# Optimization experiments

Hardware: AMD Instinct MI355X
Metric: run time of the kernel (lower is better)

The kernel has to match this reference:

```python
import jax, jax.numpy as jnp
import numpy as np

B, M, N = 512, 196, 77
FEAT, NUM_CLASSES = 512, 632
TEXT_DIM, LOCAL_DIM = 768, 576
EPS_OT, MAX_ITER, THRESH = 0.1, 100, 0.01
MARGIN, LS_EPS, TEMP, BN_EPS = 0.3, 0.1, 2.0, 1e-5
W_TEACHER = W_STUDENT = W_GLOBAL = W_LOCAL = 1.0


def setup_inputs() -> dict:
    key = jax.random.key(0)
    ks = jax.random.split(key, 16)
    nrm = lambda k, s, sc=0.02: (jax.random.normal(k, s, jnp.float32) * sc)
    return {
        "text_feat": jax.random.normal(ks[0], (B, N, TEXT_DIM), jnp.float32),
        "teacher_image_raw": jax.random.normal(ks[1], (B, TEXT_DIM), jnp.float32),
        "student_global_raw": jax.random.normal(ks[2], (B, LOCAL_DIM), jnp.float32),
        "student_local_feat": jax.random.normal(ks[3], (B, M, LOCAL_DIM), jnp.float32),
        "label": jax.random.randint(ks[4], (B,), 0, NUM_CLASSES),
        "W_tv": nrm(ks[5], (FEAT, TEXT_DIM)), "b_tv": jnp.zeros((FEAT,), jnp.float32),
        "W_tt": nrm(ks[6], (LOCAL_DIM, TEXT_DIM)), "b_tt": jnp.zeros((LOCAL_DIM,), jnp.float32),
        "W_sv": nrm(ks[7], (FEAT, LOCAL_DIM)), "b_sv": jnp.zeros((FEAT,), jnp.float32),
        "tv_bn_g": jnp.ones((FEAT,), jnp.float32), "tv_bn_b": jnp.zeros((FEAT,), jnp.float32),
        "W_cls_t": nrm(ks[8], (NUM_CLASSES, FEAT)), "b_cls_t": jnp.zeros((NUM_CLASSES,), jnp.float32),
        "W_cls_s": nrm(ks[9], (NUM_CLASSES, FEAT)), "b_cls_s": jnp.zeros((NUM_CLASSES,), jnp.float32),
    }


def batchnorm_train(x, g, b):
    mu = jnp.mean(x, axis=0)
    var = jnp.var(x, axis=0)
    return (x - mu) * jax.lax.rsqrt(var + BN_EPS) * g + b


def ce_label_smooth(logits, label):
    logp = jax.nn.log_softmax(logits, axis=-1)
    onehot = jax.nn.one_hot(label, NUM_CLASSES, dtype=logits.dtype)
    q = (1.0 - LS_EPS) * onehot + LS_EPS / NUM_CLASSES
    return -jnp.mean(jnp.sum(q * logp, axis=-1))


def triplet_hard(feat, label):
    sq = jnp.sum(feat * feat, axis=1)
    d2 = sq[:, None] + sq[None, :] - 2.0 * (feat @ feat.T)
    dist = jnp.sqrt(jnp.clip(d2, 1e-12, None))
    pos = label[:, None] == label[None, :]
    dist_ap = jnp.max(jnp.where(pos, dist, -jnp.inf), axis=1)   # hardest positive
    dist_an = jnp.min(jnp.where(pos, jnp.inf, dist), axis=1)    # hardest negative
    return jnp.mean(jax.nn.relu(dist_ap - dist_an + MARGIN))    # margin ranking, y=1


def distill_kl(teacher_logits, student_logits):
    t_logp = jax.nn.log_softmax(teacher_logits / TEMP, axis=1)
    s_logp = jax.nn.log_softmax(student_logits / TEMP, axis=1)
    t = jnp.exp(t_logp)
    return jnp.sum(t * (t_logp - s_logp)) / teacher_logits.shape[0]  # batchmean


def sinkhorn(K, u, v):
    # device-side convergence check replaces torch's .item() host sync
    def cond(st):
        i, r, c, err = st
        return jnp.logical_and(i < MAX_ITER, err >= THRESH)

    def body(st):
        i, r, c, _ = st
        r0 = r
        r = u / jnp.einsum('bmn,bn->bm', K, c)
        c = v / jnp.einsum('bmn,bm->bn', K, r)
        return (i + 1, r, c, jnp.mean(jnp.abs(r - r0)))

    r = jnp.ones_like(u)
    c = jnp.ones_like(v)
    init = (jnp.int32(0), r, c, jnp.array(jnp.inf, K.dtype))
    _, r, c, _ = jax.lax.while_loop(cond, body, init)
    return r[:, :, None] * c[:, None, :] * K


def ot_loss(student_local, teacher_text):
    s = student_local / jnp.clip(jnp.linalg.norm(student_local, axis=-1, keepdims=True), 1e-12)
    t = teacher_text / jnp.clip(jnp.linalg.norm(teacher_text, axis=-1, keepdims=True), 1e-12)
    sim = jnp.einsum('bmd,bnd->bmn', s, t)
    wdist = 1.0 - sim
    xx = jnp.full((sim.shape[0], sim.shape[1]), 1.0 / sim.shape[1], sim.dtype)
    yy = jnp.full((sim.shape[0], sim.shape[2]), 1.0 / sim.shape[2], sim.dtype)
    KK = jnp.exp(-wdist / EPS_OT)
    T = jax.lax.stop_gradient(sinkhorn(KK, xx, yy))  # torch.no_grad block
    sim_op = jnp.sum(T * sim, axis=(1, 2))
    return 1.0 - jnp.mean(sim_op)


def reference(text_feat, teacher_image_raw, student_global_raw, student_local_feat,
              label, W_tv, b_tv, W_tt, b_tt, W_sv, b_sv, tv_bn_g, tv_bn_b,
              W_cls_t, b_cls_t, W_cls_s, b_cls_s):
    teacher_image_feat = batchnorm_train(teacher_image_raw @ W_tv.T + b_tv, tv_bn_g, tv_bn_b)
    teacher_text_feat = text_feat @ W_tt.T + b_tt            # (B, N, 576)
    student_global_feat = student_global_raw @ W_sv.T + b_sv  # (B, FEAT)

    teacher_logits = teacher_image_feat @ W_cls_t.T + b_cls_t
    loss_teacher = ce_label_smooth(teacher_logits, label) + triplet_hard(teacher_image_feat, label)

    student_logits = student_global_feat @ W_cls_s.T + b_cls_s
    loss_student = ce_label_smooth(student_logits, label) + triplet_hard(student_global_feat, label)

    preds = jnp.argmax(student_logits, axis=1)
    loss_global = distill_kl(teacher_logits, student_logits)
    loss_local = ot_loss(student_local_feat, teacher_text_feat)

    loss = (W_LOCAL * loss_local + W_GLOBAL * loss_global
            + W_TEACHER * loss_teacher + W_STUDENT * loss_student)
    return loss, preds
```

## Files before the change

kernel.cpp:

```cpp
#include <hip/hip_runtime.h>
#include <math.h>

#define B_     512
#define M_     196
#define N_     77
#define FEAT_  512
#define NCLS_  632
#define TDIM_  768
#define LDIM_  576
#define LS_EPS_ 0.1f
#define MARGIN_ 0.3f
#define BN_EPS_ 1e-5f
#define SINK_ITERS 12

typedef float fx4 __attribute__((ext_vector_type(4)));
typedef float fx8 __attribute__((ext_vector_type(8)));
typedef short sx8 __attribute__((ext_vector_type(8)));
typedef __bf16 bfx8 __attribute__((ext_vector_type(8)));

__device__ inline ushort f2bf(float f) {
  union { float f; uint u; } v; v.f = f;
  uint u = v.u;
  return (ushort)((u + 0x7FFFu + ((u >> 16) & 1u)) >> 16);
}
__device__ inline float bf2f(ushort b) {
  union { uint u; float f; } v; v.u = ((uint)b) << 16;
  return v.f;
}
__device__ inline sx8 cvt8(fx8 f) {
  bfx8 h = __builtin_convertvector(f, bfx8);
  return __builtin_bit_cast(sx8, h);
}
__device__ inline fx8 b2f8(sx8 s) {
  bfx8 h = __builtin_bit_cast(bfx8, s);
  return __builtin_convertvector(h, fx8);
}
__device__ inline fx4 mfma16(sx8 a, sx8 b, fx4 c) {
  return __builtin_amdgcn_mfma_f32_16x16x32_bf16(
      __builtin_bit_cast(bfx8, a), __builtin_bit_cast(bfx8, b), c, 0, 0, 0);
}
__device__ inline void gload_lds16(const void* g, void* l) {
  auto gp = (const __attribute__((address_space(1))) uint*)(uintptr_t)g;
  auto lp = (__attribute__((address_space(3))) uint*)(uintptr_t)l;
  __builtin_amdgcn_global_load_lds(gp, lp, 16, 0, 0);
}


__device__ inline void small_mfma_body(char* smem, int bx, int by,
                                       const float* __restrict__ A,
                                       const float* __restrict__ Wm,
                                       const float* __restrict__ bias,
                                       float* __restrict__ C, int N, int K) {
  ushort* ldsA = (ushort*)smem;
  ushort* ldsW = (ushort*)(smem + 4096);
  const int tid = threadIdx.x;
  const int lane = tid & 63;
  const int wv = tid >> 6;
  const int wr = wv >> 1, wc = wv & 1;
  const int row0 = by * 64;
  const int col0 = bx * 64;
  const int mt = tid >> 6;
  const int l16 = lane & 15;
  const int k8 = lane >> 4;

  const float* pA = A + (size_t)(row0 + mt * 16 + l16) * K + k8 * 8;
  int wcl = col0 + mt * 16 + l16;
  if (wcl >= N) wcl = N - 1;
  const float* pW = Wm + (size_t)wcl * K + k8 * 8;

  fx4 acc[2][2];
  const fx4 zz = {0.f, 0.f, 0.f, 0.f};
  acc[0][0] = zz; acc[0][1] = zz; acc[1][0] = zz; acc[1][1] = zz;

  sx8 ua = cvt8(*(const fx8*)pA);
  sx8 uw = cvt8(*(const fx8*)pW);
  const int NT = K >> 5;
  for (int kt = 0; kt < NT; ++kt) {
    if (kt) __syncthreads();
    *(sx8*)&ldsA[tid * 8] = ua;
    *(sx8*)&ldsW[tid * 8] = uw;
    __syncthreads();
    if (kt + 1 < NT) {
      ua = cvt8(*(const fx8*)(pA + (kt + 1) * 32));
      uw = cvt8(*(const fx8*)(pW + (kt + 1) * 32));
    }
    sx8 af[2], bf[2];
#pragma unroll
    for (int mi = 0; mi < 2; ++mi) af[mi] = *(sx8*)&ldsA[((wr * 2 + mi) * 64 + lane) * 8];
#pragma unroll
    for (int ni = 0; ni < 2; ++ni) bf[ni] = *(sx8*)&ldsW[((wc * 2 + ni) * 64 + lane) * 8];
#pragma unroll
    for (int mi = 0; mi < 2; ++mi)
#pragma unroll
      for (int ni = 0; ni < 2; ++ni) acc[mi][ni] = mfma16(af[mi], bf[ni], acc[mi][ni]);
  }
#pragma unroll
  for (int mi = 0; mi < 2; ++mi) {
    int rbase = row0 + (wr * 2 + mi) * 16 + ((lane >> 4) << 2);
#pragma unroll
    for (int ni = 0; ni < 2; ++ni) {
      int col = col0 + (wc * 2 + ni) * 16 + l16;
      if (col < N) {
        float bv = bias ? bias[col] : 0.f;
#pragma unroll
        for (int r = 0; r < 4; ++r)
          C[(size_t)(rbase + r) * N + col] = acc[mi][ni][r] + bv;
      }
    }
  }
}

__device__ inline void gemm_nt32_body(char* smem, int bx, int by,
                                      const float* __restrict__ A,
                                      const float* __restrict__ W,
                                      const float* __restrict__ bias,
                                      float* __restrict__ C, int Mr, int N, int K) {
  float (*As)[33] = (float (*)[33])smem;
  float (*Ws)[33] = (float (*)[33])(smem + 4224);
  const int tid = threadIdx.x;
  const int tx = tid & 15, ty = tid >> 4;
  const int row0 = by * 32;
  const int col0 = bx * 32;
  float acc[2][2] = {{0.f, 0.f}, {0.f, 0.f}};

  for (int k0 = 0; k0 < K; k0 += 32) {
#pragma unroll
    for (int e = tid; e < 32 * 32; e += 256) {
      int r = e / 32, c = e % 32;
      int gr = row0 + r, gc = k0 + c;
      As[r][c] = (gr < Mr && gc < K) ? A[(size_t)gr * K + gc] : 0.f;
    }
#pragma unroll
    for (int e = tid; e < 32 * 32; e += 256) {
      int r = e / 32, c = e % 32;
      int gr = col0 + r, gc = k0 + c;
      Ws[r][c] = (gr < N && gc < K) ? W[(size_t)gr * K + gc] : 0.f;
    }
    __syncthreads();
#pragma unroll
    for (int kk = 0; kk < 32; ++kk) {
      float a[2], wv[2];
#pragma unroll
      for (int i = 0; i < 2; ++i) a[i] = As[ty * 2 + i][kk];
#pragma unroll
      for (int j = 0; j < 2; ++j) wv[j] = Ws[tx * 2 + j][kk];
#pragma unroll
      for (int i = 0; i < 2; ++i)
#pragma unroll
        for (int j = 0; j < 2; ++j) acc[i][j] += a[i] * wv[j];
    }
    __syncthreads();
  }
#pragma unroll
  for (int i = 0; i < 2; ++i) {
    int gr = row0 + ty * 2 + i;
    if (gr >= Mr) continue;
#pragma unroll
    for (int j = 0; j < 2; ++j) {
      int gc = col0 + tx * 2 + j;
      if (gc >= N) continue;
      float v = acc[i][j];
      if (bias) v += bias[gc];
      C[(size_t)gr * N + gc] = v;
    }
  }
}

__device__ inline void bn_body(char* pool, int j,
                               const float* __restrict__ X, float* __restrict__ Y,
                               const float* __restrict__ g, const float* __restrict__ b) {
  const int tid = threadIdx.x;
  float* sf = (float*)pool;
  float vals[2];
  float s = 0.f, s2 = 0.f;
  int idx = 0;
  for (int i = tid; i < B_; i += 256, ++idx) {
    float v = X[(size_t)i * FEAT_ + j];
    vals[idx] = v;
    s += v; s2 += v * v;
  }
  sf[tid] = s; __syncthreads();
  for (int k = 128; k > 0; k >>= 1) { if (tid < k) sf[tid] += sf[tid + k]; __syncthreads(); }
  float mu = sf[0] * (1.f / B_); __syncthreads();
  sf[tid] = s2; __syncthreads();
  for (int k = 128; k > 0; k >>= 1) { if (tid < k) sf[tid] += sf[tid + k]; __syncthreads(); }
  float var = sf[0] * (1.f / B_) - mu * mu;
  float scale = rsqrtf(var + BN_EPS_) * g[j];
  float shift = b[j];
  idx = 0;
  for (int i = tid; i < B_; i += 256, ++idx)
    Y[(size_t)i * FEAT_ + j] = (vals[idx] - mu) * scale + shift;
}

__device__ inline void ce_kl_body(char* pool, int row,
                                  const float* __restrict__ TL,
                                  const float* __restrict__ SL,
                                  const int* __restrict__ label,
                                  float* __restrict__ acc,
                                  float* __restrict__ preds) {
  const int tid = threadIdx.x;
  const float* tp = TL + (size_t)row * NCLS_;
  const float* sp = SL + (size_t)row * NCLS_;
  float (*red)[256] = (float (*)[256])pool;
  int* ridx = (int*)(pool + 4096);
  float* sxl = (float*)(pool + 5120);

  float tv[3], sv[3];
#pragma unroll
  for (int k = 0; k < 3; ++k) {
    int j = tid + k * 256;
    tv[k] = (j < NCLS_) ? tp[j] : -INFINITY;
    sv[k] = (j < NCLS_) ? sp[j] : -INFINITY;
  }
  float mT = -INFINITY, mS = -INFINITY, sT = 0.f, sS = 0.f;
  int ai = NCLS_;
#pragma unroll
  for (int k = 0; k < 3; ++k) {
    int j = tid + k * 256;
    if (j < NCLS_) {
      mT = fmaxf(mT, tv[k]);
      sT += tv[k]; sS += sv[k];
      if (sv[k] > mS) { mS = sv[k]; ai = j; }
    }
  }
  red[0][tid] = mT; red[1][tid] = mS; red[2][tid] = sT; red[3][tid] = sS; ridx[tid] = ai;
  __syncthreads();
  for (int k = 128; k > 0; k >>= 1) {
    if (tid < k) {
      red[0][tid] = fmaxf(red[0][tid], red[0][tid + k]);
      float om = red[1][tid + k]; int oi = ridx[tid + k];
      if (om > red[1][tid] || (om == red[1][tid] && oi < ridx[tid])) { red[1][tid] = om; ridx[tid] = oi; }
      red[2][tid] += red[2][tid + k];
      red[3][tid] += red[3][tid + k];
    }
    __syncthreads();
  }
  const float MT = red[0][0], MS = red[1][0], sumT = red[2][0], sumS = red[3][0];
  const int amax = ridx[0];
  __syncthreads();
  float etr = 0.f, esr = 0.f, eth = 0.f, esh = 0.f;
#pragma unroll
  for (int k = 0; k < 3; ++k) {
    int j = tid + k * 256;
    if (j < NCLS_) {
      etr += expf(tv[k] - MT);
      esr += expf(sv[k] - MS);
      eth += expf(0.5f * (tv[k] - MT));
      esh += expf(0.5f * (sv[k] - MS));
    }
  }
  red[0][tid] = etr; red[1][tid] = esr; red[2][tid] = eth; red[3][tid] = esh;
  __syncthreads();
  for (int k = 128; k > 0; k >>= 1) {
    if (tid < k) {
      red[0][tid] += red[0][tid + k];
      red[1][tid] += red[1][tid + k];
      red[2][tid] += red[2][tid + k];
      red[3][tid] += red[3][tid + k];
    }
    __syncthreads();
  }
  const float lseT = MT + logf(red[0][0]);
  const float lseS = MS + logf(red[1][0]);
  const float ltH = 0.5f * MT + logf(red[2][0]);
  const float lsH = 0.5f * MS + logf(red[3][0]);
  __syncthreads();
  const int lab = label[row];
  float klp = 0.f;
#pragma unroll
  for (int k = 0; k < 3; ++k) {
    int j = tid + k * 256;
    if (j < NCLS_) {
      float tlp = 0.5f * tv[k] - ltH;
      float slp = 0.5f * sv[k] - lsH;
      klp += expf(tlp) * (tlp - slp);
      if (j == lab) { sxl[0] = tv[k]; sxl[1] = sv[k]; }
    }
  }
  red[0][tid] = klp;
  __syncthreads();
  for (int k = 128; k > 0; k >>= 1) {
    if (tid < k) red[0][tid] += red[0][tid + k];
    __syncthreads();
  }
  if (tid == 0) {
    float ce_t = -((1.f - LS_EPS_) * (sxl[0] - lseT) + (LS_EPS_ / NCLS_) * (sumT - NCLS_ * lseT));
    float ce_s = -((1.f - LS_EPS_) * (sxl[1] - lseS) + (LS_EPS_ / NCLS_) * (sumS - NCLS_ * lseS));
    atomicAdd(acc + 0, ce_t * (1.f / B_));
    atomicAdd(acc + 2, ce_s * (1.f / B_));
    atomicAdd(acc + 4, red[0][0] * (1.f / B_));
    preds[row] = (float)amax;
  }
}

__device__ inline void triplet_body(char* pool, int which, int i,
                                    const float* __restrict__ Gt,
                                    const float* __restrict__ Gs,
                                    const int* __restrict__ label,
                                    float* __restrict__ acc) {
  const float* G = which ? Gs : Gt;
  float* a = acc + (which ? 3 : 1);
  const int tid = threadIdx.x;
  const int li = label[i];
  float* sap = (float*)pool;
  float* san = (float*)(pool + 1024);
  const float sqi = G[(size_t)i * B_ + i];
  float ap = -INFINITY, an = INFINITY;
  for (int j = tid; j < B_; j += 256) {
    float sqj = G[(size_t)j * B_ + j];
    float d2 = sqi + sqj - 2.f * G[(size_t)i * B_ + j];
    float d = sqrtf(fmaxf(d2, 1e-12f));
    if (label[j] == li) ap = fmaxf(ap, d); else an = fminf(an, d);
  }
  sap[tid] = ap; san[tid] = an; __syncthreads();
  for (int k = 128; k > 0; k >>= 1) {
    if (tid < k) {
      sap[tid] = fmaxf(sap[tid], sap[tid + k]);
      san[tid] = fminf(san[tid], san[tid + k]);
    }
    __syncthreads();
  }
  if (tid == 0) atomicAdd(a, fmaxf(sap[0] - san[0] + MARGIN_, 0.f) * (1.f / B_));
}

#define SKLD 88
#define SKTLD 200
__device__ inline void sinkhorn_body(char* pool, int b,
                                     const ushort* __restrict__ sim,
                                     float* __restrict__ acc) {
  const int tid = threadIdx.x;
  ushort* Kb  = (ushort*)pool;
  ushort* KbT = (ushort*)(pool + 34496);
  float* r    = (float*)(pool + 65296);
  float* c    = (float*)(pool + 66080);
  float* sf   = (float*)(pool + 66432);
  float* cs1  = (float*)(pool + 67456);
  const ushort* simb = sim + (size_t)b * (M_ * N_);
  for (int e = tid; e < 196 * SKLD; e += 256) {
    int m = e / SKLD, n = e - m * SKLD;
    if (n < 77) {
      float sv = bf2f(simb[m * 77 + n]);
      ushort h = f2bf(__expf((sv - 1.f) * 10.f));
      Kb[e] = h;
      KbT[n * SKTLD + m] = h;
    } else Kb[e] = 0;
  }
  if (tid < SKLD) c[tid] = (tid < 77) ? 1.f : 0.f;
  __syncthreads();
  const float uu = 1.f / 196.f, vv = 1.f / 77.f;
  for (int it = 0; it < SINK_ITERS; ++it) {
    if (tid < 196) {
      const ushort* Km = &Kb[tid * SKLD];
      float s = 0.f;
#pragma unroll
      for (int j = 0; j < 11; ++j) {
        fx8 kf = b2f8(*(const sx8*)&Km[j * 8]);
#pragma unroll
        for (int q = 0; q < 8; ++q) s += kf[q] * c[j * 8 + q];
      }
      r[tid] = uu / s;
    }
    __syncthreads();
    if (tid < 154) {
      const int half = (tid >= 77) ? 1 : 0;
      const int n = tid - 77 * half;
      const ushort* Kn = &KbT[n * SKTLD + 96 * half];
      const int m0 = 96 * half;
      float s = 0.f;
#pragma unroll
      for (int j = 0; j < 12; ++j) {
        fx8 kf = b2f8(*(const sx8*)&Kn[j * 8]);
#pragma unroll
        for (int q = 0; q < 8; ++q) s += kf[q] * r[m0 + j * 8 + q];
      }
      if (half) {
        s += bf2f(Kn[96]) * r[192] + bf2f(Kn[97]) * r[193]
           + bf2f(Kn[98]) * r[194] + bf2f(Kn[99]) * r[195];
        cs1[n] = s;
      } else sf[n] = s;
    }
    __syncthreads();
    if (tid < 77) c[tid] = vv / (sf[tid] + cs1[tid]);
    __syncthreads();
  }
  float part = 0.f;
  for (int e = tid; e < M_ * N_; e += 256) {
    int m = e / 77, n = e - m * 77;
    part += r[m] * c[n] * bf2f(Kb[m * SKLD + n]) * bf2f(simb[e]);
  }
  sf[tid] = part; __syncthreads();
  for (int k = 128; k > 0; k >>= 1) { if (tid < k) sf[tid] += sf[tid + k]; __syncthreads(); }
  if (tid == 0) atomicAdd(acc + 5, sf[0] * (1.f / B_));
}

template<int H>
__device__ void sim_body(int b, const float* __restrict__ S, const ushort* __restrict__ T,
                         ushort* __restrict__ sim, ushort* lds, float* sinv_s, float* tinv_s) {
  constexpr int NTILE = (H == 2) ? 5 : 4;
  constexpr int NS = NTILE * 64;
  constexpr int NC = NS + 320;
  constexpr int M0 = H * 64;
  const int tid = threadIdx.x;
  const int lane = tid & 63;
  const int w = tid >> 6;

  bool val[3], isS[3];
  const float* pS[3];
  const ushort* pT[3];
  int rowi[3], cidx[3];
  bool k0lane[3];
#pragma unroll
  for (int j = 0; j < 3; ++j) {
    int c = tid + j * 256;
    cidx[j] = c;
    val[j] = (c < NC);
    isS[j] = (c < NS);
    k0lane[j] = (((c >> 4) & 3) == 0);
    if (c < NS) {
      int tile = c >> 6;
      int r = M0 + tile * 16 + (c & 15);
      int rr = r < 196 ? r : 195;
      int ks = ((c >> 4) & 3) * 8;
      pS[j] = S + ((size_t)b * M_ + rr) * LDIM_ + ks;
      rowi[j] = rr - M0;
      pT[j] = T;
    } else {
      int cc = c - NS;
      int tile = cc >> 6;
      int r = tile * 16 + (cc & 15);
      int rr = r < 77 ? r : 76;
      int ks = ((cc >> 4) & 3) * 8;
      pT[j] = T + ((size_t)b * N_ + rr) * LDIM_ + ks;
      pS[j] = S;
      rowi[j] = rr;
    }
  }

  fx8 fS[3]; sx8 tS[3];
#pragma unroll
  for (int j = 0; j < 3; ++j) {
    if (!val[j]) continue;
    if (isS[j]) fS[j] = *(const fx8*)pS[j];
    else tS[j] = *(const sx8*)pT[j];
  }

  float ss[3] = {0.f, 0.f, 0.f};
  fx4 acc[2][5];
  const fx4 zz = {0.f, 0.f, 0.f, 0.f};
#pragma unroll
  for (int i = 0; i < 2; ++i)
#pragma unroll
    for (int j = 0; j < 5; ++j) acc[i][j] = zz;

  for (int kt = 0; kt < 18; ++kt) {
    if (kt) __syncthreads();
#pragma unroll
    for (int j = 0; j < 3; ++j) {
      if (!val[j]) continue;
      if (isS[j]) {
        *(sx8*)&lds[cidx[j] * 8] = cvt8(fS[j]);
#pragma unroll
        for (int q = 0; q < 8; ++q) ss[j] += fS[j][q] * fS[j][q];
      } else {
        *(sx8*)&lds[cidx[j] * 8] = tS[j];
        fx8 tf = b2f8(tS[j]);
#pragma unroll
        for (int q = 0; q < 8; ++q) ss[j] += tf[q] * tf[q];
      }
    }
    __syncthreads();
    if (kt < 17) {
      const int ko = (kt + 1) * 32;
#pragma unroll
      for (int j = 0; j < 3; ++j) {
        if (!val[j]) continue;
        if (isS[j]) fS[j] = *(const fx8*)(pS[j] + ko);
        else tS[j] = *(const sx8*)(pT[j] + ko);
      }
    }
    sx8 bfr[5];
#pragma unroll
    for (int ni = 0; ni < 5; ++ni) bfr[ni] = *(sx8*)&lds[(NS + ni * 64 + lane) * 8];
#pragma unroll
    for (int mi = 0; mi < 2; ++mi) {
      int lt = w + mi * 4;
      if (lt < NTILE) {
        sx8 af = *(sx8*)&lds[(lt * 64 + lane) * 8];
#pragma unroll
        for (int ni = 0; ni < 5; ++ni) acc[mi][ni] = mfma16(af, bfr[ni], acc[mi][ni]);
      }
    }
  }

#pragma unroll
  for (int j = 0; j < 3; ++j) {
    if (!val[j]) continue;
    float s = ss[j];
    s += __shfl_xor(s, 16);
    s += __shfl_xor(s, 32);
    if (k0lane[j]) {
      float inv = 1.f / fmaxf(sqrtf(s), 1e-12f);
      if (isS[j]) sinv_s[rowi[j]] = inv;
      else        tinv_s[rowi[j]] = inv;
    }
  }
  __syncthreads();

#pragma unroll
  for (int mi = 0; mi < 2; ++mi) {
    int lt = w + mi * 4;
    if (lt >= NTILE) continue;
    int lrbase = lt * 16 + ((lane >> 4) << 2);
#pragma unroll
    for (int ni = 0; ni < 5; ++ni) {
      int col = ni * 16 + (lane & 15);
      if (col < 77) {
        float tv = tinv_s[col];
#pragma unroll
        for (int r = 0; r < 4; ++r) {
          int lrow = lrbase + r;
          int row = M0 + lrow;
          if (row < 196)
            sim[((size_t)b * M_ + row) * N_ + col] = f2bf(acc[mi][ni][r] * sinv_s[lrow] * tv);
        }
      }
    }
  }
}

__device__ inline void gemm128_body(char* pool, int bx, int by,
                                    const ushort* __restrict__ A,
                                    const ushort* __restrict__ Bm,
                                    const float* __restrict__ bias,
                                    ushort* __restrict__ C) {
  ushort* ldsA = (ushort*)pool;
  ushort* ldsB = (ushort*)(pool + 8192);
  const int tid = threadIdx.x;
  const int lane = tid & 63;
  const int w = tid >> 6;
  const int wr = w >> 1, wc = w & 1;
  const int row0 = by * 128;
  const int col0 = bx * 128;
  const int l16 = lane & 15, k8 = (lane >> 4) * 8;

  const ushort* gA0 = A + (size_t)(row0 + (2 * w) * 16 + l16) * TDIM_ + k8;
  const ushort* gA1 = A + (size_t)(row0 + (2 * w + 1) * 16 + l16) * TDIM_ + k8;
  const ushort* gB0 = Bm + (size_t)(col0 + (2 * w) * 16 + l16) * TDIM_ + k8;
  const ushort* gB1 = Bm + (size_t)(col0 + (2 * w + 1) * 16 + l16) * TDIM_ + k8;
  ushort* lA0 = &ldsA[(2 * w) * 512];
  ushort* lA1 = &ldsA[(2 * w + 1) * 512];
  ushort* lB0 = &ldsB[(2 * w) * 512];
  ushort* lB1 = &ldsB[(2 * w + 1) * 512];

  fx4 acc[4][4];
  const fx4 zz = {0.f, 0.f, 0.f, 0.f};
#pragma unroll
  for (int i = 0; i < 4; ++i)
#pragma unroll
    for (int j = 0; j < 4; ++j) acc[i][j] = zz;

  for (int kt = 0; kt < 24; ++kt) {
    if (kt) __syncthreads();
    const int ko = kt * 32;
    gload_lds16(gA0 + ko, lA0);
    gload_lds16(gA1 + ko, lA1);
    gload_lds16(gB0 + ko, lB0);
    gload_lds16(gB1 + ko, lB1);
    asm volatile("s_waitcnt vmcnt(0)" ::: "memory");
    __syncthreads();
    sx8 af[4], bf[4];
#pragma unroll
    for (int mi = 0; mi < 4; ++mi) af[mi] = *(sx8*)&ldsA[((wr * 4 + mi) * 64 + lane) * 8];
#pragma unroll
    for (int ni = 0; ni < 4; ++ni) bf[ni] = *(sx8*)&ldsB[((wc * 4 + ni) * 64 + lane) * 8];
#pragma unroll
    for (int mi = 0; mi < 4; ++mi)
#pragma unroll
      for (int ni = 0; ni < 4; ++ni) acc[mi][ni] = mfma16(af[mi], bf[ni], acc[mi][ni]);
  }

#pragma unroll
  for (int mi = 0; mi < 4; ++mi) {
    int rbase = row0 + wr * 64 + mi * 16 + ((lane >> 4) << 2);
#pragma unroll
    for (int ni = 0; ni < 4; ++ni) {
      int col = col0 + wc * 64 + ni * 16 + l16;
      if (col < 576) {
        float bv = bias[col];
#pragma unroll
        for (int r = 0; r < 4; ++r)
          C[(size_t)(rbase + r) * 576 + col] = f2bf(acc[mi][ni][r] + bv);
      }
    }
  }
}


__global__ __launch_bounds__(256) void kernel_A(const float* __restrict__ t_img_raw,
                                                const float* __restrict__ W_tv,
                                                const float* __restrict__ b_tv,
                                                float* __restrict__ tlin,
                                                const float* __restrict__ s_glob_raw,
                                                const float* __restrict__ W_sv,
                                                const float* __restrict__ b_sv,
                                                float* __restrict__ sglob,
                                                const float* __restrict__ W_tt,
                                                ushort* __restrict__ Wbuf,
                                                float* __restrict__ acc,
                                                const float* __restrict__ text_feat,
                                                ushort* __restrict__ Abuf) {
  __shared__ __align__(16) char pool[8448];
  const int bid = blockIdx.x;
  const int tid = threadIdx.x;
  if (bid < 64) {
    small_mfma_body(pool, bid & 7, bid >> 3, t_img_raw, W_tv, b_tv, tlin, FEAT_, TDIM_);
  } else if (bid < 320) {
    int i = bid - 64;
    gemm_nt32_body(pool, i & 15, i >> 4, s_glob_raw, W_sv, b_sv, sglob, 512, FEAT_, LDIM_);
  } else if (bid < 561) {
    int pbid = bid - 320;
    if (pbid == 240) {
      if (tid < 8) acc[tid] = 0.f;
      return;
    }
    int i = pbid * 256 + tid;
    int row = i / 96;
    if (row < 576) {
      fx8 f = *(const fx8*)(W_tt + (size_t)i * 8);
      *(sx8*)(Wbuf + (size_t)i * 8) = cvt8(f);
    } else {
      sx8 z = {0, 0, 0, 0, 0, 0, 0, 0};
      *(sx8*)(Wbuf + (size_t)i * 8) = z;
    }
  } else {
    size_t i = (size_t)(bid - 561) * 256 + tid;
    fx8 f = *(const fx8*)(text_feat + i * 8);
    *(sx8*)(Abuf + i * 8) = cvt8(f);
  }
}

__global__ __launch_bounds__(256) void kernel_B(const ushort* __restrict__ Abuf,
                                                const ushort* __restrict__ Wbuf,
                                                const float* __restrict__ b_tt,
                                                ushort* __restrict__ ttext,
                                                const float* __restrict__ tlin,
                                                float* __restrict__ timg,
                                                const float* __restrict__ bn_g,
                                                const float* __restrict__ bn_b) {
  __shared__ __align__(16) char pool[16384];
  const int bid = blockIdx.x;
  if (bid < 1540) {
    const int xcd = bid & 7, wi = bid >> 3;
    const int swz = (xcd < 4 ? xcd * 193 : 772 + (xcd - 4) * 192) + wi;
    const int by = swz / 5, bx = swz - by * 5;
    gemm128_body(pool, bx, by, Abuf, Wbuf, b_tt, ttext);
  } else {
    bn_body(pool, bid - 1540, tlin, timg, bn_g, bn_b);
  }
}

__global__ __launch_bounds__(256) void kernel_C(const float* __restrict__ s_local,
                                                const ushort* __restrict__ ttext,
                                                ushort* __restrict__ sim,
                                                const float* __restrict__ timg,
                                                const float* __restrict__ W_ct,
                                                const float* __restrict__ b_ct,
                                                float* __restrict__ tlog,
                                                const float* __restrict__ sglob,
                                                const float* __restrict__ W_cs,
                                                const float* __restrict__ b_cs,
                                                float* __restrict__ slog,
                                                float* __restrict__ gram_t,
                                                float* __restrict__ gram_s) {
  __shared__ __align__(16) char pool[10880];
  const int bid = blockIdx.x;
  if (bid < 1536) {
    ushort* lds = (ushort*)pool;
    float* sinv_s = (float*)(pool + 10240);
    float* tinv_s = (float*)(pool + 10560);
    const int swz = (bid & 7) * 192 + (bid >> 3);
    const int b = swz / 3;
    const int q = swz - b * 3;
    if (q == 0)      sim_body<0>(b, s_local, ttext, sim, lds, sinv_s, tinv_s);
    else if (q == 1) sim_body<1>(b, s_local, ttext, sim, lds, sinv_s, tinv_s);
    else             sim_body<2>(b, s_local, ttext, sim, lds, sinv_s, tinv_s);
  } else {
    int i = bid - 1536;
    if (i < 80) {
      small_mfma_body(pool, i % 10, i / 10, timg, W_ct, b_ct, tlog, NCLS_, FEAT_);
    } else if (i < 400) {
      int j = i - 80;
      gemm_nt32_body(pool, j % 20, j / 20, sglob, W_cs, b_cs, slog, 512, NCLS_, FEAT_);
    } else if (i < 464) {
      int j = i - 400;
      small_mfma_body(pool, j & 7, j >> 3, timg, timg, nullptr, gram_t, 512, FEAT_);
    } else {
      int j = i - 464;
      small_mfma_body(pool, j & 7, j >> 3, sglob, sglob, nullptr, gram_s, 512, LDIM_);
    }
  }
}

__global__ __launch_bounds__(256) void kernel_D(const ushort* __restrict__ sim,
                                                const float* __restrict__ tlog,
                                                const float* __restrict__ slog,
                                                const float* __restrict__ gram_t,
                                                const float* __restrict__ gram_s,
                                                const int* __restrict__ label,
                                                float* __restrict__ acc,
                                                float* __restrict__ out) {
  __shared__ __align__(16) char pool[67840];
  const int bid = blockIdx.x;
  if (bid < 512) {
    sinkhorn_body(pool, bid, sim, acc);
  } else if (bid < 1024) {
    ce_kl_body(pool, bid - 512, tlog, slog, label, acc, out + 1);
  } else {
    int i = bid - 1024;
    triplet_body(pool, i >> 9, i & 511, gram_t, gram_s, label, acc);
  }
  if (threadIdx.x == 0) {
    __threadfence();
    uint prev = atomicAdd((uint*)(acc + 6), 1u);
    if (prev == 2047u) {
      float a0 = atomicAdd(acc + 0, 0.f);
      float a1 = atomicAdd(acc + 1, 0.f);
      float a2 = atomicAdd(acc + 2, 0.f);
      float a3 = atomicAdd(acc + 3, 0.f);
      float a4 = atomicAdd(acc + 4, 0.f);
      float a5 = atomicAdd(acc + 5, 0.f);
      out[0] = a0 + a1 + a2 + a3 + a4 + (1.f - a5);
    }
  }
}

extern "C" void kernel_launch(void* const* d_in, const int* in_sizes, int n_in,
                              void* d_out, int out_size, void* d_ws, size_t ws_size,
                              hipStream_t stream) {
  const float* text_feat  = (const float*)d_in[0];
  const float* t_img_raw  = (const float*)d_in[1];
  const float* s_glob_raw = (const float*)d_in[2];
  const float* s_local    = (const float*)d_in[3];
  const int*   label      = (const int*)d_in[4];
  const float* W_tv = (const float*)d_in[5];
  const float* b_tv = (const float*)d_in[6];
  const float* W_tt = (const float*)d_in[7];
  const float* b_tt = (const float*)d_in[8];
  const float* W_sv = (const float*)d_in[9];
  const float* b_sv = (const float*)d_in[10];
  const float* bn_g = (const float*)d_in[11];
  const float* bn_b = (const float*)d_in[12];
  const float* W_ct = (const float*)d_in[13];
  const float* b_ct = (const float*)d_in[14];
  const float* W_cs = (const float*)d_in[15];
  const float* b_cs = (const float*)d_in[16];
  float* out = (float*)d_out;
  float* ws = (float*)d_ws;

  float* tlin   = ws;
  float* timg   = tlin + 262144;
  float* sglob  = timg + 262144;
  float* tlog   = sglob + 262144;
  float* slog   = tlog + 323584;
  float* gram_t = slog + 323584;
  float* gram_s = gram_t + 262144;
  float* acc    = gram_s + 262144;
  ushort* Wbuf  = (ushort*)(acc + 8);
  ushort* ttext = Wbuf + 491520;
  ushort* Abuf  = ttext + 22708224;
  ushort* sim   = Abuf;

  dim3 blk(256);

  kernel_A<<<15345, blk, 0, stream>>>(t_img_raw, W_tv, b_tv, tlin,
                                      s_glob_raw, W_sv, b_sv, sglob,
                                      W_tt, Wbuf, acc, text_feat, Abuf);
  kernel_B<<<2052, blk, 0, stream>>>(Abuf, Wbuf, b_tt, ttext, tlin, timg, bn_g, bn_b);
  kernel_C<<<2064, blk, 0, stream>>>(s_local, ttext, sim,
                                     timg, W_ct, b_ct, tlog,
                                     sglob, W_cs, b_cs, slog, gram_t, gram_s);
  kernel_D<<<2048, blk, 0, stream>>>(sim, tlog, slog, gram_t, gram_s, label, acc, out);
}
```

Measured before the change: 408.2 us.

## Compute per-batch similarity in one block with text tile staged in LDS

The similarity GEMM used to be split over three blocks per batch item. It now runs in a single block per batch item. The text features are staged into LDS in two K-halves using direct global-to-LDS loads, and the student local features stream straight from global memory into registers for the MFMA. The text row norms are computed once per block. This cuts redundant text loads across blocks and the per-K-step LDS round trips and barriers. In exchange the grid has fewer blocks, LDS use grows to about 46KB, and the S loads are no longer prefetched, so occupancy and latency hiding may suffer.

```diff
diff --git a/kernel.cpp b/kernel.cpp
--- a/kernel.cpp
+++ b/kernel.cpp
@@ -393,135 +393,99 @@
   if (tid == 0) atomicAdd(acc + 5, sf[0] * (1.f / B_));
 }
 
-template<int H>
-__device__ void sim_body(int b, const float* __restrict__ S, const ushort* __restrict__ T,
-                         ushort* __restrict__ sim, ushort* lds, float* sinv_s, float* tinv_s) {
-  constexpr int NTILE = (H == 2) ? 5 : 4;
-  constexpr int NS = NTILE * 64;
-  constexpr int NC = NS + 320;
-  constexpr int M0 = H * 64;
+__device__ void sim_batch_body(int b, const float* __restrict__ S,
+                               const ushort* __restrict__ T,
+                               ushort* __restrict__ sim, char* pool) {
+  ushort* ldsT = (ushort*)pool;
+  float* tinv_s = (float*)(pool + 46080);
   const int tid = threadIdx.x;
   const int lane = tid & 63;
   const int w = tid >> 6;
-
-  bool val[3], isS[3];
-  const float* pS[3];
-  const ushort* pT[3];
-  int rowi[3], cidx[3];
-  bool k0lane[3];
-#pragma unroll
-  for (int j = 0; j < 3; ++j) {
-    int c = tid + j * 256;
-    cidx[j] = c;
-    val[j] = (c < NC);
-    isS[j] = (c < NS);
-    k0lane[j] = (((c >> 4) & 3) == 0);
-    if (c < NS) {
-      int tile = c >> 6;
-      int r = M0 + tile * 16 + (c & 15);
-      int rr = r < 196 ? r : 195;
-      int ks = ((c >> 4) & 3) * 8;
-      pS[j] = S + ((size_t)b * M_ + rr) * LDIM_ + ks;
-      rowi[j] = rr - M0;
-      pT[j] = T;
-    } else {
-      int cc = c - NS;
-      int tile = cc >> 6;
-      int r = tile * 16 + (cc & 15);
-      int rr = r < 77 ? r : 76;
-      int ks = ((cc >> 4) & 3) * 8;
-      pT[j] = T + ((size_t)b * N_ + rr) * LDIM_ + ks;
-      pS[j] = S;
-      rowi[j] = rr;
-    }
-  }
-
-  fx8 fS[3]; sx8 tS[3];
-#pragma unroll
-  for (int j = 0; j < 3; ++j) {
-    if (!val[j]) continue;
-    if (isS[j]) fS[j] = *(const fx8*)pS[j];
-    else tS[j] = *(const sx8*)pT[j];
-  }
-
-  float ss[3] = {0.f, 0.f, 0.f};
-  fx4 acc[2][5];
+  const int l16 = lane & 15;
+  const int khi = lane >> 4;
+  const float* Sb = S + (size_t)b * M_ * LDIM_;
+  const ushort* Tb = T + (size_t)b * N_ * LDIM_;
+
+  fx4 acc[4][5];
   const fx4 zz = {0.f, 0.f, 0.f, 0.f};
 #pragma unroll
-  for (int i = 0; i < 2; ++i)
-#pragma unroll
-    for (int j = 0; j < 5; ++j) acc[i][j] = zz;
-
-  for (int kt = 0; kt < 18; ++kt) {
-    if (kt) __syncthreads();
-#pragma unroll
-    for (int j = 0; j < 3; ++j) {
-      if (!val[j]) continue;
-      if (isS[j]) {
-        *(sx8*)&lds[cidx[j] * 8] = cvt8(fS[j]);
-#pragma unroll
-        for (int q = 0; q < 8; ++q) ss[j] += fS[j][q] * fS[j][q];
-      } else {
-        *(sx8*)&lds[cidx[j] * 8] = tS[j];
-        fx8 tf = b2f8(tS[j]);
-#pragma unroll
-        for (int q = 0; q < 8; ++q) ss[j] += tf[q] * tf[q];
+  for (int s = 0; s < 4; ++s)
+#pragma unroll
+    for (int ni = 0; ni < 5; ++ni) acc[s][ni] = zz;
+  float ss[4] = {0.f, 0.f, 0.f, 0.f};
+
+#pragma unroll
+  for (int p = 0; p < 2; ++p) {
+#pragma unroll
+    for (int j = 0; j < 12; ++j) {
+      int c = tid + j * 256;
+      if (c < 2880) {
+        int ktl = c / 320;
+        int rem = c - ktl * 320;
+        int nt = rem >> 6, cl = rem & 63;
+        int row = nt * 16 + (cl & 15);
+        if (row > 76) row = 76;
+        int k = (p * 9 + ktl) * 32 + ((cl >> 4) & 3) * 8;
+        gload_lds16(Tb + (size_t)row * LDIM_ + k, ldsT + (size_t)c * 8);
       }
     }
-    __syncthreads();
-    if (kt < 17) {
-      const int ko = (kt + 1) * 32;
-#pragma unroll
-      for (int j = 0; j < 3; ++j) {
-        if (!val[j]) continue;
-        if (isS[j]) fS[j] = *(const fx8*)(pS[j] + ko);
-        else tS[j] = *(const sx8*)(pT[j] + ko);
+    if (p == 0) {
+      for (int row = w; row < N_; row += 4) {
+        const ushort* x = Tb + (size_t)row * LDIM_;
+        float s = 0.f;
+#pragma unroll
+        for (int i = 0; i < 9; ++i) { float v = bf2f(x[lane + i * 64]); s += v * v; }
+#pragma unroll
+        for (int off = 32; off > 0; off >>= 1) s += __shfl_down(s, off);
+        if (lane == 0) tinv_s[row] = 1.f / fmaxf(sqrtf(s), 1e-12f);
       }
     }
-    sx8 bfr[5];
-#pragma unroll
-    for (int ni = 0; ni < 5; ++ni) bfr[ni] = *(sx8*)&lds[(NS + ni * 64 + lane) * 8];
-#pragma unroll
-    for (int mi = 0; mi < 2; ++mi) {
-      int lt = w + mi * 4;
-      if (lt < NTILE) {
-        sx8 af = *(sx8*)&lds[(lt * 64 + lane) * 8];
-#pragma unroll
-        for (int ni = 0; ni < 5; ++ni) acc[mi][ni] = mfma16(af, bfr[ni], acc[mi][ni]);
+    asm volatile("s_waitcnt vmcnt(0)" ::: "memory");
+    __syncthreads();
+
+#pragma unroll
+    for (int s = 0; s < 4; ++s) {
+      const int mt = w + s * 4;
+      if (mt >= 13) continue;
+      int row = mt * 16 + l16;
+      if (row > 195) row = 195;
+      const float* pS = Sb + (size_t)row * LDIM_ + khi * 8;
+#pragma unroll
+      for (int ktl = 0; ktl < 9; ++ktl) {
+        fx8 fa = *(const fx8*)(pS + (p * 9 + ktl) * 32);
+#pragma unroll
+        for (int q = 0; q < 8; ++q) ss[s] += fa[q] * fa[q];
+        sx8 a = cvt8(fa);
+#pragma unroll
+        for (int ni = 0; ni < 5; ++ni) {
+          sx8 bfr = *(sx8*)&ldsT[((ktl * 5 + ni) * 64 + lane) * 8];
+          acc[s][ni] = mfma16(a, bfr, acc[s][ni]);
+        }
       }
     }
-  }
-
-#pragma unroll
-  for (int j = 0; j < 3; ++j) {
-    if (!val[j]) continue;
-    float s = ss[j];
-    s += __shfl_xor(s, 16);
-    s += __shfl_xor(s, 32);
-    if (k0lane[j]) {
-      float inv = 1.f / fmaxf(sqrtf(s), 1e-12f);
-      if (isS[j]) sinv_s[rowi[j]] = inv;
-      else        tinv_s[rowi[j]] = inv;
-    }
-  }
-  __syncthreads();
-
-#pragma unroll
-  for (int mi = 0; mi < 2; ++mi) {
-    int lt = w + mi * 4;
-    if (lt >= NTILE) continue;
-    int lrbase = lt * 16 + ((lane >> 4) << 2);
-#pragma unroll
-    for (int ni = 0; ni < 5; ++ni) {
-      int col = ni * 16 + (lane & 15);
-      if (col < 77) {
-        float tv = tinv_s[col];
-#pragma unroll
-        for (int r = 0; r < 4; ++r) {
-          int lrow = lrbase + r;
-          int row = M0 + lrow;
-          if (row < 196)
-            sim[((size_t)b * M_ + row) * N_ + col] = f2bf(acc[mi][ni][r] * sinv_s[lrow] * tv);
+    if (p == 0) __syncthreads();
+  }
+
+#pragma unroll
+  for (int s = 0; s < 4; ++s) {
+    const int mt = w + s * 4;
+    if (mt >= 13) continue;
+    float sum = ss[s];
+    sum += __shfl_xor(sum, 16);
+    sum += __shfl_xor(sum, 32);
+#pragma unroll
+    for (int r = 0; r < 4; ++r) {
+      int lr = (khi << 2) + r;
+      float rs = __shfl(sum, (w << 6 & 0) + lr + (lane & ~63));
+      rs = __shfl(sum, lr);
+      float sinv = 1.f / fmaxf(sqrtf(rs), 1e-12f);
+      int grow = mt * 16 + lr;
+      if (grow < 196) {
+#pragma unroll
+        for (int ni = 0; ni < 5; ++ni) {
+          int col = ni * 16 + l16;
+          if (col < 77)
+            sim[((size_t)b * M_ + grow) * N_ + col] = f2bf(acc[s][ni][r] * sinv * tinv_s[col]);
         }
       }
     }
@@ -672,20 +636,12 @@
                                                 float* __restrict__ slog,
                                                 float* __restrict__ gram_t,
                                                 float* __restrict__ gram_s) {
-  __shared__ __align__(16) char pool[10880];
+  __shared__ __align__(16) char pool[46400];
   const int bid = blockIdx.x;
-  if (bid < 1536) {
-    ushort* lds = (ushort*)pool;
-    float* sinv_s = (float*)(pool + 10240);
-    float* tinv_s = (float*)(pool + 10560);
-    const int swz = (bid & 7) * 192 + (bid >> 3);
-    const int b = swz / 3;
-    const int q = swz - b * 3;
-    if (q == 0)      sim_body<0>(b, s_local, ttext, sim, lds, sinv_s, tinv_s);
-    else if (q == 1) sim_body<1>(b, s_local, ttext, sim, lds, sinv_s, tinv_s);
-    else             sim_body<2>(b, s_local, ttext, sim, lds, sinv_s, tinv_s);
+  if (bid < 512) {
+    sim_batch_body(bid, s_local, ttext, sim, pool);
   } else {
-    int i = bid - 1536;
+    int i = bid - 512;
     if (i < 80) {
       small_mfma_body(pool, i % 10, i / 10, timg, W_ct, b_ct, tlog, NCLS_, FEAT_);
     } else if (i < 400) {
@@ -776,7 +732,7 @@
                                       s_glob_raw, W_sv, b_sv, sglob,
                                       W_tt, Wbuf, acc, text_feat, Abuf);
   kernel_B<<<2052, blk, 0, stream>>>(Abuf, Wbuf, b_tt, ttext, tlin, timg, bn_g, bn_b);
-  kernel_C<<<2064, blk, 0, stream>>>(s_local, ttext, sim,
+  kernel_C<<<1040, blk, 0, stream>>>(s_local, ttext, sim,
                                      timg, W_ct, b_ct, tlog,
                                      sglob, W_cs, b_cs, slog, gram_t, gram_s);
   kernel_D<<<2048, blk, 0, stream>>>(sim, tlog, slog, gram_t, gram_s, label, acc, out);
```

Result: no change. 411.2 us (+0.7%).
